# Kernel tuning notes

Hardware: AMD Instinct MI355X
Metric: run time of the kernel (lower is better)

Reference implementation:

```python
import jax, jax.numpy as jnp
import numpy as np


def setup_inputs() -> dict:
    key = jax.random.key(0)
    k1, k2, k3, k4 = jax.random.split(key, 4)
    B, C, N, K, OUT = 2, 64, 50000, 9, 64
    x = jax.random.normal(k1, (B, C, N, 1), dtype=jnp.float32)
    edge_index = jax.random.randint(k2, (2, B, N, K), 0, N, dtype=jnp.int64)
    W1 = jax.random.normal(k3, (C, C), dtype=jnp.float32) * (1.0 / np.sqrt(C))
    b1 = jnp.zeros((C,), dtype=jnp.float32)
    W2 = jax.random.normal(k4, (OUT, 2 * C), dtype=jnp.float32) * (1.0 / np.sqrt(2 * C))
    b2 = jnp.zeros((OUT,), dtype=jnp.float32)
    return {"x": x, "edge_index": edge_index, "W1": W1, "b1": b1, "W2": W2, "b2": b2}


def _gather_neighbors(x_sq, idx):
    # x_sq: [B, C, N], idx: [B, N, K] -> [B, C, N, K]
    B, C, N = x_sq.shape
    K = idx.shape[-1]
    flat = jax.vmap(lambda xb, ib: xb[:, ib])(x_sq, idx.reshape(B, N * K))
    return flat.reshape(B, C, N, K)


def reference(x, edge_index, W1, b1, W2, b2):
    # x: [B, C, N, 1]; edge_index[0]: [B, N, K] neighbor indices
    x_sq = x[..., 0]                                   # [B, C, N]
    x_j = _gather_neighbors(x_sq, edge_index[0])       # [B, C, N, K]
    # nn1: 1x1 conv (per-node linear over channels) + ReLU
    h = jax.nn.relu(jnp.einsum('bcnk,dc->bdnk', x_j, W1) + b1[None, :, None, None])
    x_j_max = jnp.max(h, axis=-1, keepdims=True)       # [B, C, N, 1]
    cat = jnp.concatenate([x, x_j_max], axis=1)        # [B, 2C, N, 1]
    # nn2: 1x1 conv + ReLU
    out = jax.nn.relu(jnp.einsum('bcnk,dc->bdnk', cat, W2) + b2[None, :, None, None])
    return out                                          # [B, OUT, N, 1]
```

## Files before the change

kernel.cpp:

```cpp
#include <hip/hip_runtime.h>
#include <cstddef>

typedef unsigned int uint;
typedef _Float16 v8h __attribute__((ext_vector_type(8)));
typedef float v4f __attribute__((ext_vector_type(4)));
typedef __fp16 fp16v2 __attribute__((ext_vector_type(2)));
typedef unsigned short us2v __attribute__((ext_vector_type(2)));

union U32H2 { uint u; fp16v2 g; us2v s; };
union Frag8 { uint4 u4; uint u[4]; v8h h; };

__device__ __forceinline__ uint pkh2(float a, float b) {
  U32H2 v; v.g = __builtin_amdgcn_cvt_pkrtz(a, b); return v.u;
}
__device__ __forceinline__ uint hmax2u(uint a, uint b) {
  U32H2 x, y, r; x.u = a; y.u = b;
  r.s = __builtin_elementwise_max(x.s, y.s);
  return r.u;
}

__global__ __launch_bounds__(256, 6) void k1_node_mlp(
    const float* __restrict__ x, const float* __restrict__ W1,
    const float* __restrict__ b1, uint* __restrict__ y, int N)
{
  __shared__ __align__(16) uint xlds[64 * 36];
  const int t = threadIdx.x;
  const int nblk = (N + 63) >> 6;
  const int b = blockIdx.x / nblk;
  const int n0 = (blockIdx.x % nblk) << 6;
  const int lane = t & 63;
  const int w = t >> 6;
  const int node = t >> 2;
  const int cg = t & 3;

  {
    const bool valid = (n0 + node) < N;
    const float* xp = x + (size_t)b * 64 * N + n0 + node;
    float xv[16];
#pragma unroll
    for (int i = 0; i < 16; ++i)
      xv[i] = valid ? xp[(size_t)(cg * 16 + i) * N] : 0.0f;
    uint4 p0, p1;
    p0.x = pkh2(xv[0], xv[1]);   p0.y = pkh2(xv[2], xv[3]);
    p0.z = pkh2(xv[4], xv[5]);   p0.w = pkh2(xv[6], xv[7]);
    p1.x = pkh2(xv[8], xv[9]);   p1.y = pkh2(xv[10], xv[11]);
    p1.z = pkh2(xv[12], xv[13]); p1.w = pkh2(xv[14], xv[15]);
    uint* dst = xlds + node * 36 + cg * 8;
    *(uint4*)dst = p0;
    *(uint4*)(dst + 4) = p1;
  }

  Frag8 af[2];
  {
    const int d_row = w * 16 + (lane & 15);
    const int kb = (lane >> 4) * 8;
    const float* wp = W1 + d_row * 64 + kb;
#pragma unroll
    for (int kk = 0; kk < 2; ++kk) {
      const float4 fa = *(const float4*)(wp + kk * 32);
      const float4 fb = *(const float4*)(wp + kk * 32 + 4);
      af[kk].u4.x = pkh2(fa.x, fa.y);
      af[kk].u4.y = pkh2(fa.z, fa.w);
      af[kk].u4.z = pkh2(fb.x, fb.y);
      af[kk].u4.w = pkh2(fb.z, fb.w);
    }
  }
  __syncthreads();

  const int q = lane >> 4;
  const int cidx = lane & 15;
  v4f acc[4];
  {
    v4f bi;
#pragma unroll
    for (int r = 0; r < 4; ++r) bi[r] = b1[w * 16 + q * 4 + r];
#pragma unroll
    for (int nt = 0; nt < 4; ++nt) acc[nt] = bi;
  }
#pragma unroll
  for (int nt = 0; nt < 4; ++nt) {
#pragma unroll
    for (int kk = 0; kk < 2; ++kk) {
      Frag8 bf;
      bf.u4 = *(const uint4*)(xlds + (nt * 16 + cidx) * 36 + kk * 16 + q * 4);
      acc[nt] = __builtin_amdgcn_mfma_f32_16x16x32_f16(af[kk].h, bf.h, acc[nt], 0, 0, 0);
    }
  }

#pragma unroll
  for (int nt = 0; nt < 4; ++nt) {
    const int n = n0 + nt * 16 + cidx;
    if (n < N) {
      uint2 v;
      v.x = pkh2(fmaxf(acc[nt][0], 0.f), fmaxf(acc[nt][1], 0.f));
      v.y = pkh2(fmaxf(acc[nt][2], 0.f), fmaxf(acc[nt][3], 0.f));
      *(uint2*)(y + ((size_t)b * N + n) * 32 + w * 8 + q * 2) = v;
    }
  }
}

__global__ __launch_bounds__(256, 4) void k2_gather_out(
    const float* __restrict__ x, const int* __restrict__ eidx,
    const uint* __restrict__ y, const float* __restrict__ W2,
    const float* __restrict__ b2, float* __restrict__ out,
    int N, int K, int nblk_pad)
{
  __shared__ __align__(16) uint blds[64 * 68];
  const int t = threadIdx.x;
  const int nblk = (N + 63) >> 6;
  const int g = blockIdx.x;
  const int slot = g & 7;
  const int b = slot >> 2;
  const int tile = ((g >> 3) << 2) + (slot & 3);
  if (tile >= nblk) return;
  const int n0 = tile << 6;
  const int lane = t & 63;
  const int w = t >> 6;
  const int node = t >> 2;
  const int cg = t & 3;
  const int n = n0 + node;

  const bool is64 = (__ballot(eidx[2 * lane + 1] == 0) == ~0ull);

  int jj[9];
  const bool act = (n < N) && (K == 9);
  if (act) {
    const size_t r = (size_t)b * N + n;
    if (is64) {
      const uint2* p = (const uint2*)eidx + r * 9;
#pragma unroll
      for (int k = 0; k < 9; ++k) jj[k] = (int)p[k].x;
    } else {
      const int* p = eidx + r * 9;
#pragma unroll
      for (int k = 0; k < 9; ++k) jj[k] = p[k];
    }
  }

  {
    const bool valid = n < N;
    const float* xp = x + (size_t)b * 64 * N + n0 + node;
    float xv[16];
#pragma unroll
    for (int i = 0; i < 16; ++i)
      xv[i] = valid ? xp[(size_t)(cg * 16 + i) * N] : 0.0f;
    uint4 p0, p1;
    p0.x = pkh2(xv[0], xv[1]);   p0.y = pkh2(xv[2], xv[3]);
    p0.z = pkh2(xv[4], xv[5]);   p0.w = pkh2(xv[6], xv[7]);
    p1.x = pkh2(xv[8], xv[9]);   p1.y = pkh2(xv[10], xv[11]);
    p1.z = pkh2(xv[12], xv[13]); p1.w = pkh2(xv[14], xv[15]);
    uint* dst = blds + node * 68 + cg * 8;
    *(uint4*)dst = p0;
    *(uint4*)(dst + 4) = p1;
  }

  Frag8 af[4];
  {
    const int o_row = w * 16 + (lane & 15);
    const int kb = (lane >> 4) * 8;
    const float* wp = W2 + o_row * 128 + kb;
#pragma unroll
    for (int kk = 0; kk < 4; ++kk) {
      const float4 fa = *(const float4*)(wp + kk * 32);
      const float4 fb = *(const float4*)(wp + kk * 32 + 4);
      af[kk].u4.x = pkh2(fa.x, fa.y);
      af[kk].u4.y = pkh2(fa.z, fa.w);
      af[kk].u4.z = pkh2(fb.x, fb.y);
      af[kk].u4.w = pkh2(fb.z, fb.w);
    }
  }

  uint m[8] = {0, 0, 0, 0, 0, 0, 0, 0};
  if (act) {
    const uint* yb = y + (size_t)b * N * 32 + cg * 8;
    uint4 ga[9], gb[9];
#pragma unroll
    for (int k = 0; k < 9; ++k) {
      const uint* base = yb + (size_t)jj[k] * 32;
      ga[k] = *(const uint4*)base;
      gb[k] = *(const uint4*)(base + 4);
    }
#pragma unroll
    for (int k = 0; k < 9; ++k) {
      m[0] = hmax2u(m[0], ga[k].x); m[1] = hmax2u(m[1], ga[k].y);
      m[2] = hmax2u(m[2], ga[k].z); m[3] = hmax2u(m[3], ga[k].w);
      m[4] = hmax2u(m[4], gb[k].x); m[5] = hmax2u(m[5], gb[k].y);
      m[6] = hmax2u(m[6], gb[k].z); m[7] = hmax2u(m[7], gb[k].w);
    }
  } else if (n < N) {
    const size_t r = (size_t)b * N + n;
    const uint* yb = y + (size_t)b * N * 32 + cg * 8;
    for (int k = 0; k < K; ++k) {
      const int j = is64 ? (int)((const uint2*)eidx + r * K)[k].x
                         : (eidx + r * K)[k];
      const uint* base = yb + (size_t)j * 32;
      const uint4 a0 = *(const uint4*)base, a1 = *(const uint4*)(base + 4);
      m[0] = hmax2u(m[0], a0.x); m[1] = hmax2u(m[1], a0.y);
      m[2] = hmax2u(m[2], a0.z); m[3] = hmax2u(m[3], a0.w);
      m[4] = hmax2u(m[4], a1.x); m[5] = hmax2u(m[5], a1.y);
      m[6] = hmax2u(m[6], a1.z); m[7] = hmax2u(m[7], a1.w);
    }
  }
  {
    uint* dst = blds + node * 68 + 32 + cg * 8;
    uint4 v0; v0.x = m[0]; v0.y = m[1]; v0.z = m[2]; v0.w = m[3];
    uint4 v1; v1.x = m[4]; v1.y = m[5]; v1.z = m[6]; v1.w = m[7];
    *(uint4*)dst = v0;
    *(uint4*)(dst + 4) = v1;
  }
  __syncthreads();

  const int q = lane >> 4;
  const int cidx = lane & 15;
  const int o0 = w * 16;
  v4f acc[4];
  {
    v4f bi;
#pragma unroll
    for (int r = 0; r < 4; ++r) bi[r] = b2[o0 + q * 4 + r];
#pragma unroll
    for (int nt = 0; nt < 4; ++nt) acc[nt] = bi;
  }
#pragma unroll
  for (int nt = 0; nt < 4; ++nt) {
#pragma unroll
    for (int kk = 0; kk < 4; ++kk) {
      Frag8 bf;
      bf.u4 = *(const uint4*)(blds + (nt * 16 + cidx) * 68 + kk * 16 + q * 4);
      acc[nt] = __builtin_amdgcn_mfma_f32_16x16x32_f16(af[kk].h, bf.h, acc[nt], 0, 0, 0);
    }
  }

#pragma unroll
  for (int nt = 0; nt < 4; ++nt) {
    const int nn = n0 + nt * 16 + cidx;
    if (nn < N) {
#pragma unroll
      for (int r = 0; r < 4; ++r) {
        const int o = o0 + q * 4 + r;
        out[(size_t)(b * 64 + o) * N + nn] = fmaxf(acc[nt][r], 0.f);
      }
    }
  }
}

extern "C" void kernel_launch(void* const* d_in, const int* in_sizes, int n_in,
                              void* d_out, int out_size, void* d_ws, size_t ws_size,
                              hipStream_t stream) {
  const float* x  = (const float*)d_in[0];
  const int*   ei = (const int*)d_in[1];
  const float* W1 = (const float*)d_in[2];
  const float* b1 = (const float*)d_in[3];
  const float* W2 = (const float*)d_in[4];
  const float* b2 = (const float*)d_in[5];
  float* out = (float*)d_out;

  const int N = in_sizes[0] / 128;
  const int K = in_sizes[1] / (4 * N);

  uint* y = (uint*)d_ws;

  const int nblk = (N + 63) >> 6;
  const int nblk_pad = (nblk + 3) & ~3;
  k1_node_mlp<<<2 * nblk, 256, 0, stream>>>(x, W1, b1, y, N);
  k2_gather_out<<<2 * nblk_pad, 256, 0, stream>>>(x, ei, y, W2, b2, out, N, K, nblk_pad);
}
```

Baseline: 119.1 us.

## Interleave fp16 node features with MLP output into per-node records

The first kernel now also writes the fp16-packed input features for each node into a per-node 256-byte record, next to the hidden activations. The second kernel reads that contiguous fp16 row instead of re-reading strided fp32 x. The neighbor gather is split into two passes so fewer registers are live at once, and the batch-interleaved block ordering is replaced by a plain linear mapping. The trade-off is a doubled gathered working set in L2, plus extra writes in the first kernel. Out-of-range tail nodes may also read slightly past the record buffer; their outputs are masked.

```diff
diff --git a/kernel.cpp b/kernel.cpp
--- a/kernel.cpp
+++ b/kernel.cpp
@@ -19,9 +19,10 @@
   return r.u;
 }
 
+
 __global__ __launch_bounds__(256, 6) void k1_node_mlp(
     const float* __restrict__ x, const float* __restrict__ W1,
-    const float* __restrict__ b1, uint* __restrict__ y, int N)
+    const float* __restrict__ b1, uint* __restrict__ rec, int N)
 {
   __shared__ __align__(16) uint xlds[64 * 36];
   const int t = threadIdx.x;
@@ -32,14 +33,14 @@
   const int w = t >> 6;
   const int node = t >> 2;
   const int cg = t & 3;
-
-  {
-    const bool valid = (n0 + node) < N;
+  const bool nvalid = (n0 + node) < N;
+
+  {
     const float* xp = x + (size_t)b * 64 * N + n0 + node;
     float xv[16];
 #pragma unroll
     for (int i = 0; i < 16; ++i)
-      xv[i] = valid ? xp[(size_t)(cg * 16 + i) * N] : 0.0f;
+      xv[i] = nvalid ? xp[(size_t)(cg * 16 + i) * N] : 0.0f;
     uint4 p0, p1;
     p0.x = pkh2(xv[0], xv[1]);   p0.y = pkh2(xv[2], xv[3]);
     p0.z = pkh2(xv[4], xv[5]);   p0.w = pkh2(xv[6], xv[7]);
@@ -48,6 +49,11 @@
     uint* dst = xlds + node * 36 + cg * 8;
     *(uint4*)dst = p0;
     *(uint4*)(dst + 4) = p1;
+    if (nvalid) {
+      uint* rx = rec + ((size_t)b * N + n0 + node) * 64 + cg * 8;
+      *(uint4*)rx = p0;
+      *(uint4*)(rx + 4) = p1;
+    }
   }
 
   Frag8 af[2];
@@ -94,26 +100,22 @@
       uint2 v;
       v.x = pkh2(fmaxf(acc[nt][0], 0.f), fmaxf(acc[nt][1], 0.f));
       v.y = pkh2(fmaxf(acc[nt][2], 0.f), fmaxf(acc[nt][3], 0.f));
-      *(uint2*)(y + ((size_t)b * N + n) * 32 + w * 8 + q * 2) = v;
+      *(uint2*)(rec + ((size_t)b * N + n) * 64 + 32 + w * 8 + q * 2) = v;
     }
   }
 }
 
 __global__ __launch_bounds__(256, 4) void k2_gather_out(
     const float* __restrict__ x, const int* __restrict__ eidx,
-    const uint* __restrict__ y, const float* __restrict__ W2,
-    const float* __restrict__ b2, float* __restrict__ out,
-    int N, int K, int nblk_pad)
+    const uint* __restrict__ rec, const float* __restrict__ W2,
+    const float* __restrict__ b2, float* __restrict__ out, int N, int K)
 {
   __shared__ __align__(16) uint blds[64 * 68];
   const int t = threadIdx.x;
   const int nblk = (N + 63) >> 6;
   const int g = blockIdx.x;
-  const int slot = g & 7;
-  const int b = slot >> 2;
-  const int tile = ((g >> 3) << 2) + (slot & 3);
-  if (tile >= nblk) return;
-  const int n0 = tile << 6;
+  const int b = (g >= nblk) ? 1 : 0;
+  const int n0 = (g - b * nblk) << 6;
   const int lane = t & 63;
   const int w = t >> 6;
   const int node = t >> 2;
@@ -138,17 +140,9 @@
   }
 
   {
-    const bool valid = n < N;
-    const float* xp = x + (size_t)b * 64 * N + n0 + node;
-    float xv[16];
-#pragma unroll
-    for (int i = 0; i < 16; ++i)
-      xv[i] = valid ? xp[(size_t)(cg * 16 + i) * N] : 0.0f;
-    uint4 p0, p1;
-    p0.x = pkh2(xv[0], xv[1]);   p0.y = pkh2(xv[2], xv[3]);
-    p0.z = pkh2(xv[4], xv[5]);   p0.w = pkh2(xv[6], xv[7]);
-    p1.x = pkh2(xv[8], xv[9]);   p1.y = pkh2(xv[10], xv[11]);
-    p1.z = pkh2(xv[12], xv[13]); p1.w = pkh2(xv[14], xv[15]);
+    const uint* rx = rec + ((size_t)b * N + n0 + node) * 64 + cg * 8;
+    const uint4 p0 = *(const uint4*)rx;
+    const uint4 p1 = *(const uint4*)(rx + 4);
     uint* dst = blds + node * 68 + cg * 8;
     *(uint4*)dst = p0;
     *(uint4*)(dst + 4) = p1;
@@ -172,28 +166,31 @@
 
   uint m[8] = {0, 0, 0, 0, 0, 0, 0, 0};
   if (act) {
-    const uint* yb = y + (size_t)b * N * 32 + cg * 8;
-    uint4 ga[9], gb[9];
-#pragma unroll
-    for (int k = 0; k < 9; ++k) {
-      const uint* base = yb + (size_t)jj[k] * 32;
-      ga[k] = *(const uint4*)base;
-      gb[k] = *(const uint4*)(base + 4);
-    }
+    const uint* yb = rec + (size_t)b * N * 64 + 32 + cg * 8;
+    uint4 ga[9];
+#pragma unroll
+    for (int k = 0; k < 9; ++k)
+      ga[k] = *(const uint4*)(yb + (size_t)jj[k] * 64);
 #pragma unroll
     for (int k = 0; k < 9; ++k) {
       m[0] = hmax2u(m[0], ga[k].x); m[1] = hmax2u(m[1], ga[k].y);
       m[2] = hmax2u(m[2], ga[k].z); m[3] = hmax2u(m[3], ga[k].w);
-      m[4] = hmax2u(m[4], gb[k].x); m[5] = hmax2u(m[5], gb[k].y);
-      m[6] = hmax2u(m[6], gb[k].z); m[7] = hmax2u(m[7], gb[k].w);
+    }
+#pragma unroll
+    for (int k = 0; k < 9; ++k)
+      ga[k] = *(const uint4*)(yb + (size_t)jj[k] * 64 + 4);
+#pragma unroll
+    for (int k = 0; k < 9; ++k) {
+      m[4] = hmax2u(m[4], ga[k].x); m[5] = hmax2u(m[5], ga[k].y);
+      m[6] = hmax2u(m[6], ga[k].z); m[7] = hmax2u(m[7], ga[k].w);
     }
   } else if (n < N) {
     const size_t r = (size_t)b * N + n;
-    const uint* yb = y + (size_t)b * N * 32 + cg * 8;
+    const uint* yb = rec + (size_t)b * N * 64 + 32 + cg * 8;
     for (int k = 0; k < K; ++k) {
       const int j = is64 ? (int)((const uint2*)eidx + r * K)[k].x
                          : (eidx + r * K)[k];
-      const uint* base = yb + (size_t)j * 32;
+      const uint* base = yb + (size_t)j * 64;
       const uint4 a0 = *(const uint4*)base, a1 = *(const uint4*)(base + 4);
       m[0] = hmax2u(m[0], a0.x); m[1] = hmax2u(m[1], a0.y);
       m[2] = hmax2u(m[2], a0.z); m[3] = hmax2u(m[3], a0.w);
@@ -258,10 +255,9 @@
   const int N = in_sizes[0] / 128;
   const int K = in_sizes[1] / (4 * N);
 
-  uint* y = (uint*)d_ws;
+  uint* rec = (uint*)d_ws;
 
   const int nblk = (N + 63) >> 6;
-  const int nblk_pad = (nblk + 3) & ~3;
-  k1_node_mlp<<<2 * nblk, 256, 0, stream>>>(x, W1, b1, y, N);
-  k2_gather_out<<<2 * nblk_pad, 256, 0, stream>>>(x, ei, y, W2, b2, out, N, K, nblk_pad);
-}
+  k1_node_mlp<<<2 * nblk, 256, 0, stream>>>(x, W1, b1, rec, N);
+  k2_gather_out<<<2 * nblk, 256, 0, stream>>>(x, ei, rec, W2, b2, out, N, K);
+}
```

Result: no change. 117.9 us (-1.0%).
